# Performance work log

Hardware: AMD Instinct MI355X
Metric: run time of the kernel (lower is better)

## Reference

```python
import jax, jax.numpy as jnp
import numpy as np

N, D, H, L = 100000, 128, 4, 2
C = D // H  # per-head channels
E = 1600000
NEG_SLOPE = 0.2
LN_EPS = 1e-5


def setup_inputs() -> dict:
    key = jax.random.key(0)
    ks = jax.random.split(key, 8)
    x = jax.random.normal(ks[0], (N, D), dtype=jnp.float32)
    edge_index = jax.random.randint(ks[1], (2, E), 0, N, dtype=jnp.int64)
    s = 1.0 / np.sqrt(D)
    Wl = jax.random.normal(ks[2], (L, D, D), dtype=jnp.float32) * s
    Wr = jax.random.normal(ks[3], (L, D, D), dtype=jnp.float32) * s
    att = jax.random.normal(ks[4], (L, H, C), dtype=jnp.float32) * (1.0 / np.sqrt(C))
    bias = jnp.zeros((L, D), dtype=jnp.float32)
    gamma = jnp.ones((L, D), dtype=jnp.float32)
    beta = jnp.zeros((L, D), dtype=jnp.float32)
    return {"x": x, "edge_index": edge_index, "Wl": Wl, "Wr": Wr,
            "att": att, "bias": bias, "gamma": gamma, "beta": beta}


def _gatv2_layer(h, src, dst, Wl, Wr, att, bias):
    # h: (N, D); src/dst: (E2,) with self-loops already appended
    xl = (h @ Wl).reshape(N, H, C)  # source-side transform
    xr = (h @ Wr).reshape(N, H, C)  # target-side transform
    e = jax.nn.leaky_relu(xl[src] + xr[dst], NEG_SLOPE)      # (E2, H, C)
    alpha = jnp.einsum('ehc,hc->eh', e, att)                 # (E2, H)
    # segment softmax over incoming edges of each destination node
    m = jax.ops.segment_max(alpha, dst, num_segments=N)      # (N, H)
    ea = jnp.exp(alpha - m[dst])
    s = jax.ops.segment_sum(ea, dst, num_segments=N)         # (N, H)
    a = ea / s[dst]                                          # (E2, H)
    out = jax.ops.segment_sum(a[:, :, None] * xl[src], dst, num_segments=N)
    return out.reshape(N, D) + bias


def _layer_norm(y, gamma, beta):
    mu = jnp.mean(y, axis=-1, keepdims=True)
    var = jnp.var(y, axis=-1, keepdims=True)
    return (y - mu) * jax.lax.rsqrt(var + LN_EPS) * gamma + beta


def reference(x, edge_index, Wl, Wr, att, bias, gamma, beta):
    # PyG GATv2Conv defaults: add_self_loops=True (eval mode: dropouts identity)
    loops = jnp.arange(N, dtype=edge_index.dtype)
    src = jnp.concatenate([edge_index[0], loops])
    dst = jnp.concatenate([edge_index[1], loops])
    h = x
    for l in range(L):
        g = _gatv2_layer(h, src, dst, Wl[l], Wr[l], att[l], bias[l])
        h = h + jax.nn.elu(_layer_norm(g, gamma[l], beta[l]))
    return h
```

## Files before the change

kernel.cpp:

```cpp
#include <hip/hip_runtime.h>
#include <hip/hip_fp16.h>
#include <math.h>

#define N_NODES 100000
#define D_FEAT  128
#define E_EDGES 1600000
#define E2      (E_EDGES + N_NODES)
#define NEG_SLOPE 0.2f
#define LN_EPS    1e-5f

#define NB   391
#define TS   8192
#define NTIL ((E2 + TS - 1) / TS)

typedef __attribute__((ext_vector_type(8))) short short8;
typedef __attribute__((ext_vector_type(4))) float floatx4;
typedef _Float16 h2 __attribute__((ext_vector_type(2)));

static __device__ __forceinline__ float fdot2f(h2 a, h2 b, float c) {
#if __has_builtin(__builtin_amdgcn_fdot2)
    return __builtin_amdgcn_fdot2(a, b, c, false);
#else
    return (float)a[0] * (float)b[0] + (float)a[1] * (float)b[1] + c;
#endif
}

__global__ __launch_bounds__(1024) void tile_count(const int* __restrict__ edge_dst,
                                                   int* __restrict__ tcnt) {
    __shared__ int h[NB];
    const int t = threadIdx.x;
    if (t < NB) h[t] = 0;
    __syncthreads();
    const int base = blockIdx.x * TS;
#pragma unroll
    for (int j = 0; j < TS / 1024; ++j) {
        int i = base + j * 1024 + t;
        if (i < E2) {
            int d = (i < E_EDGES) ? edge_dst[i] : (i - E_EDGES);
            atomicAdd(&h[d >> 8], 1);
        }
    }
    __syncthreads();
    if (t < NB) tcnt[blockIdx.x * NB + t] = h[t];
}

__global__ __launch_bounds__(256) void col_scan(const int* __restrict__ tcnt,
                                                int* __restrict__ toff,
                                                int* __restrict__ bcnt) {
    __shared__ int s[256];
    const int b = blockIdx.x;
    const int t = threadIdx.x;
    int v = (t < NTIL) ? tcnt[t * NB + b] : 0;
    s[t] = v;
    __syncthreads();
    for (int off = 1; off < 256; off <<= 1) {
        int x = (t >= off) ? s[t - off] : 0;
        __syncthreads();
        s[t] += x;
        __syncthreads();
    }
    if (t < NTIL) toff[t * NB + b] = s[t] - v;
    if (t == 255) bcnt[b] = s[255];
}

__global__ __launch_bounds__(512) void bucket_scan(const int* __restrict__ bcnt,
                                                   int* __restrict__ bstart,
                                                   int* __restrict__ rowstart) {
    __shared__ int s[512];
    const int t = threadIdx.x;
    int v = (t < NB) ? bcnt[t] : 0;
    s[t] = v;
    __syncthreads();
    for (int off = 1; off < 512; off <<= 1) {
        int x = (t >= off) ? s[t - off] : 0;
        __syncthreads();
        s[t] += x;
        __syncthreads();
    }
    if (t <= NB) bstart[t] = s[t] - v;
    if (t == 0) rowstart[N_NODES] = E2;
}

__global__ __launch_bounds__(1024) void tile_scatter(const int* __restrict__ edge_src,
                                                     const int* __restrict__ edge_dst,
                                                     const int* __restrict__ bstart,
                                                     const int* __restrict__ toff,
                                                     unsigned* __restrict__ pairbuf) {
    __shared__ int base[NB];
    __shared__ int cur[NB];
    const int t = threadIdx.x;
    if (t < NB) { base[t] = bstart[t] + toff[blockIdx.x * NB + t]; cur[t] = 0; }
    __syncthreads();
    const int tb = blockIdx.x * TS;
#pragma unroll
    for (int j = 0; j < TS / 1024; ++j) {
        int i = tb + j * 1024 + t;
        if (i < E2) {
            int d, sr;
            if (i < E_EDGES) { d = edge_dst[i]; sr = edge_src[i]; }
            else             { d = i - E_EDGES; sr = d; }
            int b = d >> 8;
            int rank = atomicAdd(&cur[b], 1);
            pairbuf[base[b] + rank] = (unsigned)sr | ((unsigned)(d & 255) << 17);
        }
    }
}

__global__ __launch_bounds__(1024) void bucketize(const unsigned* __restrict__ pairbuf,
                                                  const int* __restrict__ bstart,
                                                  int* __restrict__ rowstart,
                                                  int* __restrict__ csr_src) {
    __shared__ int cnt[256], sc[256], cur[256];
    const int blk = blockIdx.x;
    const int t = threadIdx.x;
    const int nbase = blk << 8;
    if (t < 256) cnt[t] = 0;
    __syncthreads();
    const int e0 = bstart[blk], e1 = bstart[blk + 1];
    for (int p = e0 + t; p < e1; p += 1024)
        atomicAdd(&cnt[pairbuf[p] >> 17], 1);
    __syncthreads();
    int v = (t < 256) ? cnt[t] : 0;
    if (t < 256) sc[t] = v;
    __syncthreads();
    for (int off = 1; off < 256; off <<= 1) {
        int x = (t < 256 && t >= off) ? sc[t - off] : 0;
        __syncthreads();
        if (t < 256) sc[t] += x;
        __syncthreads();
    }
    if (t < 256) {
        int excl = sc[t] - v;
        int node = nbase + t;
        if (node < N_NODES) rowstart[node] = e0 + excl;
        cur[t] = e0 + excl;
    }
    __syncthreads();
    for (int p = e0 + t; p < e1; p += 1024) {
        unsigned pr = pairbuf[p];
        int pos = atomicAdd(&cur[pr >> 17], 1);
        csr_src[pos] = (int)(pr & 0x1FFFF);
    }
}

static __device__ __forceinline__ unsigned short f2bf(float f) {
    unsigned u = __float_as_uint(f);
    unsigned r = (u + 0x7fffu + ((u >> 16) & 1u)) >> 16;
    return (unsigned short)r;
}

__global__ void prep_wt(const float* __restrict__ Wl, const float* __restrict__ Wr,
                        const float* __restrict__ att,
                        unsigned short* __restrict__ Wt, _Float16* __restrict__ atth) {
    int idx = blockIdx.x * 256 + threadIdx.x;
    if (idx < 65536) {
        int l    = idx >> 15;
        int rem  = idx & 32767;
        int side = rem >> 14;
        int cw   = rem & 16383;
        int col  = cw >> 7, k = cw & 127;
        const float* W = side ? Wr : Wl;
        Wt[idx] = f2bf(W[l * 16384 + k * 128 + col]);
    } else if (idx < 65536 + 256) {
        int j = idx - 65536;
        atth[j] = (_Float16)att[j];
    }
}

__global__ __launch_bounds__(256) void gemm_mfma2(
        const unsigned short* __restrict__ hbf,
        const float* __restrict__ Afp,
        const unsigned short* __restrict__ Wt,
        _Float16* __restrict__ xl, _Float16* __restrict__ xr, int n_rows) {
    const int wave = threadIdx.x >> 6;
    const int lane = threadIdx.x & 63;
    const int m = lane & 15;
    const int q = lane >> 4;
    const int r0 = (blockIdx.x * 4 + wave) * 32;

    int arow0 = r0 + m;        if (arow0 >= n_rows) arow0 = n_rows - 1;
    int arow1 = r0 + 16 + m;   if (arow1 >= n_rows) arow1 = n_rows - 1;

    floatx4 acc[2][2][8];
#pragma unroll
    for (int s = 0; s < 2; ++s)
#pragma unroll
        for (int rt = 0; rt < 2; ++rt)
#pragma unroll
            for (int ct = 0; ct < 8; ++ct) acc[s][rt][ct] = (floatx4){0.f,0.f,0.f,0.f};

#pragma unroll
    for (int ks = 0; ks < 4; ++ks) {
        const int k0 = ks * 32 + q * 8;
        short8 a0, a1;
        if (Afp) {
            float4 f0 = *(const float4*)(Afp + (size_t)arow0 * 128 + k0);
            float4 f1 = *(const float4*)(Afp + (size_t)arow0 * 128 + k0 + 4);
            float4 g0 = *(const float4*)(Afp + (size_t)arow1 * 128 + k0);
            float4 g1 = *(const float4*)(Afp + (size_t)arow1 * 128 + k0 + 4);
            a0 = (short8){(short)f2bf(f0.x), (short)f2bf(f0.y), (short)f2bf(f0.z), (short)f2bf(f0.w),
                          (short)f2bf(f1.x), (short)f2bf(f1.y), (short)f2bf(f1.z), (short)f2bf(f1.w)};
            a1 = (short8){(short)f2bf(g0.x), (short)f2bf(g0.y), (short)f2bf(g0.z), (short)f2bf(g0.w),
                          (short)f2bf(g1.x), (short)f2bf(g1.y), (short)f2bf(g1.z), (short)f2bf(g1.w)};
        } else {
            a0 = *(const short8*)(hbf + (size_t)arow0 * 128 + k0);
            a1 = *(const short8*)(hbf + (size_t)arow1 * 128 + k0);
        }
#pragma unroll
        for (int s = 0; s < 2; ++s) {
#pragma unroll
            for (int ct = 0; ct < 8; ++ct) {
                short8 b = *(const short8*)(Wt + (size_t)s * 16384
                                            + (size_t)(ct * 16 + m) * 128 + k0);
                acc[s][0][ct] = __builtin_amdgcn_mfma_f32_16x16x32_bf16(a0, b, acc[s][0][ct], 0, 0, 0);
                acc[s][1][ct] = __builtin_amdgcn_mfma_f32_16x16x32_bf16(a1, b, acc[s][1][ct], 0, 0, 0);
            }
        }
    }

#pragma unroll
    for (int s = 0; s < 2; ++s) {
        _Float16* out = s ? xr : xl;
#pragma unroll
        for (int rt = 0; rt < 2; ++rt)
#pragma unroll
            for (int ct = 0; ct < 8; ++ct)
#pragma unroll
                for (int i = 0; i < 4; ++i) {
                    int row = r0 + rt * 16 + q * 4 + i;
                    if (row < n_rows)
                        out[(size_t)row * 128 + ct * 16 + m] = (_Float16)acc[s][rt][ct][i];
                }
    }
}

union U16 { uint4 u; h2 h[4]; };

__global__ __launch_bounds__(256) void gat_node6(
        const _Float16* __restrict__ xl,
        const _Float16* __restrict__ xr,
        const float* __restrict__ h_in,
        const int* __restrict__ rowstart, const int* __restrict__ csr_src,
        const _Float16* __restrict__ atth, const float* __restrict__ bias,
        const float* __restrict__ gamma, const float* __restrict__ beta,
        float* __restrict__ h_out, unsigned* __restrict__ hbf_out) {
    __shared__ float lacc[4][8 * 136];
    __shared__ float lS[4][4];

    const int wave = threadIdx.x >> 6;
    const int lane = threadIdx.x & 63;
    const int node = blockIdx.x * 4 + wave;
    const int esub = lane >> 3;
    const int r    = lane & 7;
    const int c0   = r * 16;

    U16 xra, xrb, ata, atb;
    {
        const uint4* xp = (const uint4*)(xr + (size_t)node * 128 + c0);
        xra.u = xp[0]; xrb.u = xp[1];
        const uint4* ap = (const uint4*)(atth + c0);
        ata.u = ap[0]; atb.u = ap[1];
    }
    const h2 ns2 = {(_Float16)NEG_SLOPE, (_Float16)NEG_SLOPE};

    const int p0 = rowstart[node], p1 = rowstart[node + 1];
    float s = 0.f;
    h2 acc2[8];
#pragma unroll
    for (int j = 0; j < 8; ++j) acc2[j] = (h2){(_Float16)0.f, (_Float16)0.f};

    const unsigned short* xls = (const unsigned short*)xl;

    int pb = p0;
    bool vA = (p0 + esub) < p1;
    U16 a0, a1, b0, b1;
    {
        int pc = vA ? (p0 + esub) : (p1 - 1);
        int src = csr_src[pc];
        const uint4* rp = (const uint4*)(xls + (size_t)src * 128 + c0);
        a0.u = rp[0]; a1.u = rp[1];
    }
    bool vB = false;
    if (p0 + 8 < p1) {
        vB = (p0 + 8 + esub) < p1;
        int pc = vB ? (p0 + 8 + esub) : (p1 - 1);
        int src = csr_src[pc];
        const uint4* rp = (const uint4*)(xls + (size_t)src * 128 + c0);
        b0.u = rp[0]; b1.u = rp[1];
    }

    while (pb < p1) {
        U16 c0v, c1v;
        bool vC = false;
        if (pb + 16 < p1) {
            vC = (pb + 16 + esub) < p1;
            int pc = vC ? (pb + 16 + esub) : (p1 - 1);
            int src = csr_src[pc];
            const uint4* rp = (const uint4*)(xls + (size_t)src * 128 + c0);
            c0v.u = rp[0]; c1v.u = rp[1];
        }

        float d = 0.f;
#pragma unroll
        for (int qq = 0; qq < 4; ++qq) {
            h2 z  = a0.h[qq] + xra.h[qq];
            h2 lk = __builtin_elementwise_max(z, z * ns2);
            d = fdot2f(lk, ata.h[qq], d);
        }
#pragma unroll
        for (int qq = 0; qq < 4; ++qq) {
            h2 z  = a1.h[qq] + xrb.h[qq];
            h2 lk = __builtin_elementwise_max(z, z * ns2);
            d = fdot2f(lk, atb.h[qq], d);
        }
        float alpha = d + __shfl_xor(d, 1);
        float w = vA ? __expf(alpha) : 0.f;
        s += w;
        h2 w2 = {(_Float16)w, (_Float16)w};
#pragma unroll
        for (int qq = 0; qq < 4; ++qq)
            acc2[qq] = w2 * a0.h[qq] + acc2[qq];
#pragma unroll
        for (int qq = 0; qq < 4; ++qq)
            acc2[qq + 4] = w2 * a1.h[qq] + acc2[qq + 4];

        a0 = b0; a1 = b1; vA = vB;
        b0 = c0v; b1 = c1v; vB = vC;
        pb += 8;
    }

    float ssum = s;
    ssum += __shfl_xor(ssum, 8);
    ssum += __shfl_xor(ssum, 16);
    ssum += __shfl_xor(ssum, 32);

    float* lb = &lacc[wave][esub * 136 + c0];
#pragma unroll
    for (int qq = 0; qq < 4; ++qq) {
        h2 lo = acc2[2 * qq], hi = acc2[2 * qq + 1];
        float4 o = {(float)lo[0], (float)lo[1], (float)hi[0], (float)hi[1]};
        *(float4*)(lb + 4 * qq) = o;
    }
    if (esub == 0 && (r & 1) == 0) lS[wave][r >> 1] = ssum;

    const int c = lane * 2;
    float S = lS[wave][lane >> 4];
    float g0 = 0.f, g1 = 0.f;
#pragma unroll
    for (int e = 0; e < 8; ++e) {
        float2 f = *(const float2*)(&lacc[wave][e * 136 + c]);
        g0 += f.x; g1 += f.y;
    }
    const float invS = 1.f / S;
    g0 = g0 * invS + bias[c];
    g1 = g1 * invS + bias[c + 1];

    float sum = g0 + g1, sq = g0 * g0 + g1 * g1;
#pragma unroll
    for (int off = 1; off < 64; off <<= 1) {
        sum += __shfl_xor(sum, off);
        sq  += __shfl_xor(sq, off);
    }
    float mu   = sum * (1.f / 128.f);
    float var  = sq * (1.f / 128.f) - mu * mu;
    float rstd = rsqrtf(var + LN_EPS);
    float y0 = (g0 - mu) * rstd * gamma[c]     + beta[c];
    float y1 = (g1 - mu) * rstd * gamma[c + 1] + beta[c + 1];
    float e0 = (y0 > 0.f) ? y0 : (__expf(y0) - 1.f);
    float e1 = (y1 > 0.f) ? y1 : (__expf(y1) - 1.f);

    const float2 hv = *(const float2*)(h_in + (size_t)node * 128 + c);
    float2 o;
    o.x = hv.x + e0;
    o.y = hv.y + e1;
    *(float2*)(h_out + (size_t)node * 128 + c) = o;
    if (hbf_out) {
        unsigned pk = (unsigned)f2bf(o.x) | ((unsigned)f2bf(o.y) << 16);
        hbf_out[(size_t)node * 64 + lane] = pk;
    }
}

extern "C" void kernel_launch(void* const* d_in, const int* in_sizes, int n_in,
                              void* d_out, int out_size, void* d_ws, size_t ws_size,
                              hipStream_t stream) {
    const float* x     = (const float*)d_in[0];
    const int*   eidx  = (const int*)d_in[1];
    const float* Wl    = (const float*)d_in[2];
    const float* Wr    = (const float*)d_in[3];
    const float* att   = (const float*)d_in[4];
    const float* bias  = (const float*)d_in[5];
    const float* gamma = (const float*)d_in[6];
    const float* beta  = (const float*)d_in[7];
    float* out = (float*)d_out;

    char* ws = (char*)d_ws;
    _Float16* xl = (_Float16*)ws;              ws += (size_t)N_NODES * 128 * 2;
    _Float16* xr = (_Float16*)ws;              ws += (size_t)N_NODES * 128 * 2;
    float* h1 = (float*)ws;                    ws += (size_t)N_NODES * 128 * 4;
    unsigned short* hbf = (unsigned short*)ws; ws += (size_t)N_NODES * 128 * 2;
    unsigned short* Wt  = (unsigned short*)ws; ws += (size_t)65536 * 2;
    _Float16* atth = (_Float16*)ws;            ws += 256 * 2;
    unsigned* pairbuf = (unsigned*)ws;         ws += (size_t)E2 * 4;
    int* tcnt     = (int*)ws; ws += (size_t)NTIL * NB * 4;
    int* toff     = (int*)ws; ws += (size_t)NTIL * NB * 4;
    int* bcnt     = (int*)ws; ws += (NB + 1) * 4;
    int* bstart   = (int*)ws; ws += (NB + 1) * 4;
    int* rowstart = (int*)ws; ws += (size_t)(N_NODES + 4) * 4;
    int* csr_src  = (int*)ws; ws += (size_t)E2 * 4;

    const int* edge_src = eidx;
    const int* edge_dst = eidx + E_EDGES;

    prep_wt<<<257, 256, 0, stream>>>(Wl, Wr, att, Wt, atth);

    tile_count<<<NTIL, 1024, 0, stream>>>(edge_dst, tcnt);
    col_scan<<<NB, 256, 0, stream>>>(tcnt, toff, bcnt);
    bucket_scan<<<1, 512, 0, stream>>>(bcnt, bstart, rowstart);
    tile_scatter<<<NTIL, 1024, 0, stream>>>(edge_src, edge_dst, bstart, toff, pairbuf);
    bucketize<<<NB, 1024, 0, stream>>>(pairbuf, bstart, rowstart, csr_src);

    const int gemm_gx = (N_NODES + 127) / 128;
    for (int l = 0; l < 2; ++l) {
        const float* hin  = (l == 0) ? x  : h1;
        float*       hout = (l == 1) ? out : h1;
        gemm_mfma2<<<gemm_gx, 256, 0, stream>>>(
            hbf, (l == 0) ? x : nullptr, Wt + (size_t)l * 32768, xl, xr, N_NODES);
        gat_node6<<<N_NODES / 4, 256, 0, stream>>>(
            xl, xr, hin, rowstart, csr_src,
            atth + l * 128, bias + l * 128, gamma + l * 128, beta + l * 128,
            hout, (l == 0) ? (unsigned*)hbf : nullptr);
    }
}
```

Baseline: 400.1 us.

## Fuse CSR build and weight prep into one cooperative kernel with grid syncs

Merges the six CSR-construction and weight-prep launches into one cooperative kernel that separates phases with grid-wide syncs, removing per-launch gaps and small-kernel tails. The column scan now runs as one wavefront per bucket using shuffles instead of a shared-memory block scan, and bucketize loops over buckets across the NTIL blocks. The transposed weights are also stored in a k-blocked layout so each GEMM B-fragment load reads contiguous 16-byte chunks. The cooperative launch needs all NTIL 1024-thread blocks to be co-resident, and the launch's return value is ignored.

```diff
diff --git a/kernel.cpp b/kernel.cpp
--- a/kernel.cpp
+++ b/kernel.cpp
@@ -1,6 +1,9 @@
 #include <hip/hip_runtime.h>
 #include <hip/hip_fp16.h>
+#include <hip/hip_cooperative_groups.h>
 #include <math.h>
+
+namespace cg = cooperative_groups;
 
 #define N_NODES 100000
 #define D_FEAT  128
@@ -25,145 +28,150 @@
 #endif
 }
 
-__global__ __launch_bounds__(1024) void tile_count(const int* __restrict__ edge_dst,
-                                                   int* __restrict__ tcnt) {
-    __shared__ int h[NB];
-    const int t = threadIdx.x;
-    if (t < NB) h[t] = 0;
-    __syncthreads();
-    const int base = blockIdx.x * TS;
-#pragma unroll
-    for (int j = 0; j < TS / 1024; ++j) {
-        int i = base + j * 1024 + t;
-        if (i < E2) {
-            int d = (i < E_EDGES) ? edge_dst[i] : (i - E_EDGES);
-            atomicAdd(&h[d >> 8], 1);
-        }
-    }
-    __syncthreads();
-    if (t < NB) tcnt[blockIdx.x * NB + t] = h[t];
-}
-
-__global__ __launch_bounds__(256) void col_scan(const int* __restrict__ tcnt,
-                                                int* __restrict__ toff,
-                                                int* __restrict__ bcnt) {
-    __shared__ int s[256];
-    const int b = blockIdx.x;
-    const int t = threadIdx.x;
-    int v = (t < NTIL) ? tcnt[t * NB + b] : 0;
-    s[t] = v;
-    __syncthreads();
-    for (int off = 1; off < 256; off <<= 1) {
-        int x = (t >= off) ? s[t - off] : 0;
-        __syncthreads();
-        s[t] += x;
-        __syncthreads();
-    }
-    if (t < NTIL) toff[t * NB + b] = s[t] - v;
-    if (t == 255) bcnt[b] = s[255];
-}
-
-__global__ __launch_bounds__(512) void bucket_scan(const int* __restrict__ bcnt,
-                                                   int* __restrict__ bstart,
-                                                   int* __restrict__ rowstart) {
-    __shared__ int s[512];
-    const int t = threadIdx.x;
-    int v = (t < NB) ? bcnt[t] : 0;
-    s[t] = v;
-    __syncthreads();
-    for (int off = 1; off < 512; off <<= 1) {
-        int x = (t >= off) ? s[t - off] : 0;
-        __syncthreads();
-        s[t] += x;
-        __syncthreads();
-    }
-    if (t <= NB) bstart[t] = s[t] - v;
-    if (t == 0) rowstart[N_NODES] = E2;
-}
-
-__global__ __launch_bounds__(1024) void tile_scatter(const int* __restrict__ edge_src,
-                                                     const int* __restrict__ edge_dst,
-                                                     const int* __restrict__ bstart,
-                                                     const int* __restrict__ toff,
-                                                     unsigned* __restrict__ pairbuf) {
-    __shared__ int base[NB];
-    __shared__ int cur[NB];
-    const int t = threadIdx.x;
-    if (t < NB) { base[t] = bstart[t] + toff[blockIdx.x * NB + t]; cur[t] = 0; }
-    __syncthreads();
-    const int tb = blockIdx.x * TS;
-#pragma unroll
-    for (int j = 0; j < TS / 1024; ++j) {
-        int i = tb + j * 1024 + t;
-        if (i < E2) {
-            int d, sr;
-            if (i < E_EDGES) { d = edge_dst[i]; sr = edge_src[i]; }
-            else             { d = i - E_EDGES; sr = d; }
-            int b = d >> 8;
-            int rank = atomicAdd(&cur[b], 1);
-            pairbuf[base[b] + rank] = (unsigned)sr | ((unsigned)(d & 255) << 17);
-        }
-    }
-}
-
-__global__ __launch_bounds__(1024) void bucketize(const unsigned* __restrict__ pairbuf,
-                                                  const int* __restrict__ bstart,
-                                                  int* __restrict__ rowstart,
-                                                  int* __restrict__ csr_src) {
-    __shared__ int cnt[256], sc[256], cur[256];
-    const int blk = blockIdx.x;
-    const int t = threadIdx.x;
-    const int nbase = blk << 8;
-    if (t < 256) cnt[t] = 0;
-    __syncthreads();
-    const int e0 = bstart[blk], e1 = bstart[blk + 1];
-    for (int p = e0 + t; p < e1; p += 1024)
-        atomicAdd(&cnt[pairbuf[p] >> 17], 1);
-    __syncthreads();
-    int v = (t < 256) ? cnt[t] : 0;
-    if (t < 256) sc[t] = v;
-    __syncthreads();
-    for (int off = 1; off < 256; off <<= 1) {
-        int x = (t < 256 && t >= off) ? sc[t - off] : 0;
-        __syncthreads();
-        if (t < 256) sc[t] += x;
-        __syncthreads();
-    }
-    if (t < 256) {
-        int excl = sc[t] - v;
-        int node = nbase + t;
-        if (node < N_NODES) rowstart[node] = e0 + excl;
-        cur[t] = e0 + excl;
-    }
-    __syncthreads();
-    for (int p = e0 + t; p < e1; p += 1024) {
-        unsigned pr = pairbuf[p];
-        int pos = atomicAdd(&cur[pr >> 17], 1);
-        csr_src[pos] = (int)(pr & 0x1FFFF);
-    }
-}
-
 static __device__ __forceinline__ unsigned short f2bf(float f) {
     unsigned u = __float_as_uint(f);
     unsigned r = (u + 0x7fffu + ((u >> 16) & 1u)) >> 16;
     return (unsigned short)r;
 }
 
-__global__ void prep_wt(const float* __restrict__ Wl, const float* __restrict__ Wr,
-                        const float* __restrict__ att,
-                        unsigned short* __restrict__ Wt, _Float16* __restrict__ atth) {
-    int idx = blockIdx.x * 256 + threadIdx.x;
-    if (idx < 65536) {
-        int l    = idx >> 15;
-        int rem  = idx & 32767;
-        int side = rem >> 14;
-        int cw   = rem & 16383;
-        int col  = cw >> 7, k = cw & 127;
-        const float* W = side ? Wr : Wl;
-        Wt[idx] = f2bf(W[l * 16384 + k * 128 + col]);
-    } else if (idx < 65536 + 256) {
-        int j = idx - 65536;
-        atth[j] = (_Float16)att[j];
+__global__ __launch_bounds__(1024) void csr_coop(
+        const int* __restrict__ edge_src, const int* __restrict__ edge_dst,
+        const float* __restrict__ Wl, const float* __restrict__ Wr,
+        const float* __restrict__ att,
+        unsigned short* __restrict__ Wt, _Float16* __restrict__ atth,
+        int* __restrict__ tcnt, int* __restrict__ toff, int* __restrict__ bcnt,
+        int* __restrict__ bstart, int* __restrict__ rowstart,
+        unsigned* __restrict__ pairbuf, int* __restrict__ csr_src) {
+    cg::grid_group grid = cg::this_grid();
+    __shared__ int sA[512];
+    __shared__ int sB[512];
+    __shared__ int sC[512];
+    const int t = threadIdx.x;
+    const int blk = blockIdx.x;
+
+    if (t < NB) sA[t] = 0;
+    __syncthreads();
+    {
+        const int base = blk * TS;
+#pragma unroll
+        for (int j = 0; j < TS / 1024; ++j) {
+            int i = base + j * 1024 + t;
+            if (i < E2) {
+                int d = (i < E_EDGES) ? edge_dst[i] : (i - E_EDGES);
+                atomicAdd(&sA[d >> 8], 1);
+            }
+        }
+        int gid = blk * 1024 + t;
+        for (int idx = gid; idx < 65536 + 256; idx += NTIL * 1024) {
+            if (idx < 65536) {
+                int l = idx >> 15, rem = idx & 32767, side = rem >> 14, cw = rem & 16383;
+                int col = cw >> 7, k = cw & 127;
+                const float* W = side ? Wr : Wl;
+                int kb = k >> 3, j = k & 7;
+                Wt[(size_t)((l * 2 + side) * 16 + kb) * 1024 + col * 8 + j] =
+                    f2bf(W[l * 16384 + k * 128 + col]);
+            } else {
+                int j = idx - 65536;
+                atth[j] = (_Float16)att[j];
+            }
+        }
+    }
+    __syncthreads();
+    if (t < NB) tcnt[blk * NB + t] = sA[t];
+    grid.sync();
+
+    {
+        int wv = (blk << 4) + (t >> 6);
+        int lane = t & 63;
+        if (wv < NB) {
+            const int col = wv;
+            int v[4]; int lsum = 0;
+#pragma unroll
+            for (int i = 0; i < 4; ++i) {
+                int tt = lane * 4 + i;
+                int x = (tt < NTIL) ? tcnt[tt * NB + col] : 0;
+                v[i] = lsum; lsum += x;
+            }
+            int incl = lsum;
+#pragma unroll
+            for (int off = 1; off < 64; off <<= 1) {
+                int x = __shfl_up(incl, off);
+                if (lane >= off) incl += x;
+            }
+            int excl = incl - lsum;
+#pragma unroll
+            for (int i = 0; i < 4; ++i) {
+                int tt = lane * 4 + i;
+                if (tt < NTIL) toff[tt * NB + col] = excl + v[i];
+            }
+            if (lane == 63) bcnt[col] = incl;
+        }
+    }
+    grid.sync();
+
+    if (blk == 0) {
+        int v = (t < NB) ? bcnt[t] : 0;
+        if (t < 512) sC[t] = v;
+        __syncthreads();
+        for (int off = 1; off < 512; off <<= 1) {
+            int x = (t < 512 && t >= off) ? sC[t - off] : 0;
+            __syncthreads();
+            if (t < 512) sC[t] += x;
+            __syncthreads();
+        }
+        if (t <= NB) bstart[t] = sC[t] - v;
+        if (t == 0) rowstart[N_NODES] = E2;
+    }
+    grid.sync();
+
+    {
+        if (t < NB) { sA[t] = bstart[t] + toff[blk * NB + t]; sB[t] = 0; }
+        __syncthreads();
+        const int tb = blk * TS;
+#pragma unroll
+        for (int j = 0; j < TS / 1024; ++j) {
+            int i = tb + j * 1024 + t;
+            if (i < E2) {
+                int d, sr;
+                if (i < E_EDGES) { d = edge_dst[i]; sr = edge_src[i]; }
+                else             { d = i - E_EDGES; sr = d; }
+                int b = d >> 8;
+                int rank = atomicAdd(&sB[b], 1);
+                pairbuf[sA[b] + rank] = (unsigned)sr | ((unsigned)(d & 255) << 17);
+            }
+        }
+    }
+    grid.sync();
+
+    for (int bk = blk; bk < NB; bk += NTIL) {
+        if (t < 256) sA[t] = 0;
+        __syncthreads();
+        const int e0 = bstart[bk], e1 = bstart[bk + 1];
+        for (int p = e0 + t; p < e1; p += 1024)
+            atomicAdd(&sA[pairbuf[p] >> 17], 1);
+        __syncthreads();
+        int v = (t < 256) ? sA[t] : 0;
+        if (t < 256) sB[t] = v;
+        __syncthreads();
+        for (int off = 1; off < 256; off <<= 1) {
+            int x = (t < 256 && t >= off) ? sB[t - off] : 0;
+            __syncthreads();
+            if (t < 256) sB[t] += x;
+            __syncthreads();
+        }
+        if (t < 256) {
+            int excl = sB[t] - v;
+            int node = (bk << 8) + t;
+            if (node < N_NODES) rowstart[node] = e0 + excl;
+            sC[t] = e0 + excl;
+        }
+        __syncthreads();
+        for (int p = e0 + t; p < e1; p += 1024) {
+            unsigned pr = pairbuf[p];
+            int pos = atomicAdd(&sC[pr >> 17], 1);
+            csr_src[pos] = (int)(pr & 0x1FFFF);
+        }
+        __syncthreads();
     }
 }
 
@@ -206,12 +214,13 @@
             a0 = *(const short8*)(hbf + (size_t)arow0 * 128 + k0);
             a1 = *(const short8*)(hbf + (size_t)arow1 * 128 + k0);
         }
+        const int kb = ks * 4 + q;
 #pragma unroll
         for (int s = 0; s < 2; ++s) {
 #pragma unroll
             for (int ct = 0; ct < 8; ++ct) {
-                short8 b = *(const short8*)(Wt + (size_t)s * 16384
-                                            + (size_t)(ct * 16 + m) * 128 + k0);
+                short8 b = *(const short8*)(Wt + (size_t)(s * 16 + kb) * 1024
+                                            + (ct * 16 + m) * 8);
                 acc[s][0][ct] = __builtin_amdgcn_mfma_f32_16x16x32_bf16(a0, b, acc[s][0][ct], 0, 0, 0);
                 acc[s][1][ct] = __builtin_amdgcn_mfma_f32_16x16x32_bf16(a1, b, acc[s][1][ct], 0, 0, 0);
             }
@@ -411,13 +420,14 @@
     const int* edge_src = eidx;
     const int* edge_dst = eidx + E_EDGES;
 
-    prep_wt<<<257, 256, 0, stream>>>(Wl, Wr, att, Wt, atth);
-
-    tile_count<<<NTIL, 1024, 0, stream>>>(edge_dst, tcnt);
-    col_scan<<<NB, 256, 0, stream>>>(tcnt, toff, bcnt);
-    bucket_scan<<<1, 512, 0, stream>>>(bcnt, bstart, rowstart);
-    tile_scatter<<<NTIL, 1024, 0, stream>>>(edge_src, edge_dst, bstart, toff, pairbuf);
-    bucketize<<<NB, 1024, 0, stream>>>(pairbuf, bstart, rowstart, csr_src);
+    {
+        void* args[] = {(void*)&edge_src, (void*)&edge_dst, (void*)&Wl, (void*)&Wr,
+                        (void*)&att, (void*)&Wt, (void*)&atth, (void*)&tcnt,
+                        (void*)&toff, (void*)&bcnt, (void*)&bstart, (void*)&rowstart,
+                        (void*)&pairbuf, (void*)&csr_src};
+        (void)hipLaunchCooperativeKernel((void*)csr_coop, dim3(NTIL), dim3(1024),
+                                         args, 0, stream);
+    }
 
     const int gemm_gx = (N_NODES + 127) / 128;
     for (int l = 0; l < 2; ++l) {
```

After: 503.7 us. +25.9%, slower.
